# Kernel tuning notes

Hardware: AMD Instinct MI355X
Metric: run time of the kernel (lower is better)

Reference implementation:

```python
import jax, jax.numpy as jnp
import numpy as np
from jax import lax

DN = ('NCHW', 'OIHW', 'NCHW')


def conv3x3(x, w, groups=1):
    return lax.conv_general_dilated(x, w, window_strides=(1, 1),
                                    padding=((1, 1), (1, 1)),
                                    dimension_numbers=DN,
                                    feature_group_count=groups)


def conv1x1(x, w):
    return lax.conv_general_dilated(x, w, window_strides=(1, 1),
                                    padding=((0, 0), (0, 0)),
                                    dimension_numbers=DN)


def l2_normalize(t, eps=1e-12):
    n = jnp.sqrt(jnp.sum(t * t, axis=-1, keepdims=True))
    return t / jnp.maximum(n, eps)


def setup_inputs() -> dict:
    key = jax.random.key(0)
    ks = jax.random.split(key, 10)
    B, C, H, W = 4, 64, 256, 256
    heads = 8
    s = 0.05
    return {
        'x': jax.random.normal(ks[0], (B, C, H, W), jnp.float32),
        'w_iem': jax.random.normal(ks[1], (C, C, 3, 3), jnp.float32) * s,
        'w_nem': jax.random.normal(ks[2], (C, C, 3, 3), jnp.float32) * s,
        'w_iem_dw': jax.random.normal(ks[3], (C, 1, 3, 3), jnp.float32) * s,
        'w_nem_dw': jax.random.normal(ks[4], (C, 1, 3, 3), jnp.float32) * s,
        'w_q': jax.random.normal(ks[5], (C, C, 1, 1), jnp.float32) * s,
        'w_k': jax.random.normal(ks[6], (C, C, 1, 1), jnp.float32) * s,
        'w_v': jax.random.normal(ks[7], (C, C, 1, 1), jnp.float32) * s,
        'w_proj': jax.random.normal(ks[8], (C, C, 1, 1), jnp.float32) * s,
        'temperature': jnp.ones((1, heads, 1, 1, 1, 1), jnp.float32),
    }


def igam_forward(x, w_iem, w_nem, w_iem_dw, w_nem_dw, w_q, w_k, w_v, w_proj,
                 temperature, num_heads=8, window_size=8):
    b, c, h, w = x.shape
    ws = window_size
    pad_h = (ws - h % ws) % ws
    pad_w = (ws - w % ws) % ws
    if pad_h or pad_w:  # replicate pad on right/bottom (static)
        x = jnp.pad(x, ((0, 0), (0, 0), (0, pad_h), (0, pad_w)), mode='edge')
    hp, wp = x.shape[-2:]
    heads = num_heads
    d = c // heads
    nh, nw = hp // ws, wp // ws

    illumination_map = conv3x3(jax.nn.sigmoid(conv3x3(x, w_iem)), w_iem_dw, groups=c)
    noise_map = conv3x3(jax.nn.sigmoid(conv3x3(x, w_nem)), w_nem_dw, groups=c)
    illum_scalar = jnp.mean(illumination_map, axis=1, keepdims=True)  # (b,1,hp,wp)
    noise_scalar = jnp.mean(noise_map, axis=1, keepdims=True)

    q = conv1x1(illumination_map, w_q)
    k = conv1x1(noise_map, w_k)
    v = conv1x1(x, w_v)

    def to_windows(t):  # (b,c,hp,wp) -> (b,heads,nh,nw,ws*ws,d)
        t = t.reshape(b, heads, d, hp, wp).transpose(0, 1, 3, 4, 2)
        t = t.reshape(b, heads, nh, ws, nw, ws, d).transpose(0, 1, 2, 4, 3, 5, 6)
        return t.reshape(b, heads, nh, nw, ws * ws, d)

    def scalar_to_windows(t):  # (b,1,hp,wp) -> (b,1,nh,nw,ws*ws,1)
        t = t.reshape(b, 1, nh, ws, nw, ws).transpose(0, 1, 2, 4, 3, 5)
        return t.reshape(b, 1, nh, nw, ws * ws, 1)

    qw = l2_normalize(to_windows(q)) * (1.0 + scalar_to_windows(illum_scalar))
    kw = l2_normalize(to_windows(k)) * jnp.clip(1.0 - scalar_to_windows(noise_scalar), 0.0, 1.0)
    vw = to_windows(v)

    scale = d ** (-0.5)
    attn = jnp.einsum('bhnmqd,bhnmkd->bhnmqk', qw, kw) * scale * temperature
    attn = jax.nn.softmax(attn, axis=-1)
    outw = jnp.einsum('bhnmqk,bhnmkd->bhnmqd', attn, vw)

    # merge windows back to (b, c, hp, wp)
    outw = outw.reshape(b, heads, nh, nw, ws, ws, d).transpose(0, 1, 6, 2, 4, 3, 5)
    out = outw.reshape(b, heads * d, nh * ws, nw * ws)
    if pad_h or pad_w:
        out = out[:, :, :h, :w]
    return conv1x1(out, w_proj)


def reference(x, w_iem, w_nem, w_iem_dw, w_nem_dw, w_q, w_k, w_v, w_proj,
              temperature):
    return igam_forward(x, w_iem, w_nem, w_iem_dw, w_nem_dw, w_q, w_k, w_v,
                        w_proj, temperature)
```

## Files before the change

kernel.cpp:

```cpp
#include <hip/hip_runtime.h>
#include <math.h>

#define W_ 256
#define H_ 256
#define HW 65536
#define CC 64

typedef _Float16 h16;
typedef _Float16 half8 __attribute__((ext_vector_type(8)));
typedef float f32x4  __attribute__((ext_vector_type(4)));
typedef float f32x16 __attribute__((ext_vector_type(16)));

__device__ __forceinline__ unsigned pk2(float a, float b) {
  union { h16 h[2]; unsigned u; } c;
  c.h[0] = (h16)a; c.h[1] = (h16)b;
  return c.u;
}
__device__ __forceinline__ void plswap(unsigned &a, unsigned &b) {
  asm volatile("v_permlane32_swap_b32 %0, %1" : "+v"(a), "+v"(b));
}

__global__ __launch_bounds__(256) void k_wprep(
    const float* __restrict__ wi, const float* __restrict__ wn, h16* __restrict__ Bt)
{
  int i = blockIdx.x * 256 + threadIdx.x;
  if (i >= 128 * 576) return;
  int co = i / 576, k = i - co * 576;
  int tap = k >> 6, ci = k & 63;
  const float* src = (co < 64) ? wi : wn;
  int c = co & 63;
  Bt[i] = (h16)src[(c * 64 + ci) * 9 + tap];
}

__global__ __launch_bounds__(256) void k_wprep2(
    const float* __restrict__ wq, const float* __restrict__ wk,
    const float* __restrict__ wv, const float* __restrict__ wp,
    const float* __restrict__ wdw1, const float* __restrict__ wdw2,
    h16* __restrict__ W)
{
  int i = blockIdx.x * 256 + threadIdx.x;
  if (i >= 17536) return;
  if (i < 16384) {
    int m = i >> 12, e = i & 4095;
    const float* s = (m == 0) ? wq : (m == 1) ? wk : (m == 2) ? wv : wp;
    W[i] = (h16)s[e];
  } else {
    int e = i - 16384;
    int pass = e / 576, rem = e - pass * 576;
    int tap = rem >> 6, c = rem & 63;
    const float* s = pass ? wdw2 : wdw1;
    W[i] = (h16)s[c * 9 + tap];
  }
}

__global__ __launch_bounds__(256) void k_xpose(
    const float* __restrict__ x, h16* __restrict__ xT)
{
  __shared__ __align__(16) char sm[64 * 132];
  const int tid = threadIdx.x;
  const int xt = blockIdx.x, y = blockIdx.y, b = blockIdx.z;
  const int x0 = xt * 64;
  const float* xb = x + ((size_t)b * CC) * HW + y * W_ + x0;
  const int ci = tid >> 2, q = tid & 3;
#pragma unroll
  for (int k = 0; k < 4; ++k) {
    const int pc = q + k * 4;
    float4 v = *(const float4*)(xb + (size_t)ci * HW + pc * 4);
    const int px = pc * 4;
    *(h16*)(sm + (px + 0) * 132 + ci * 2) = (h16)v.x;
    *(h16*)(sm + (px + 1) * 132 + ci * 2) = (h16)v.y;
    *(h16*)(sm + (px + 2) * 132 + ci * 2) = (h16)v.z;
    *(h16*)(sm + (px + 3) * 132 + ci * 2) = (h16)v.w;
  }
  __syncthreads();
  h16* dst = xT + (((size_t)b * 256 + y) * 256 + x0) * 64;
#pragma unroll
  for (int it = 0; it < 2; ++it) {
    int task = tid + it * 256;
    int px = task >> 3, c8 = task & 7;
    int4 d = *(const int4*)(sm + px * 132 + c8 * 16);
    *(int4*)(dst + px * 64 + c8 * 8) = d;
  }
}

__global__ __launch_bounds__(512) void k_conv3x3x2(
    const h16* __restrict__ xT, const h16* __restrict__ Bt,
    h16* __restrict__ T1, h16* __restrict__ T2)
{
  __shared__ __align__(16) char lds[38016];

  const int tid = threadIdx.x;
  const int b = blockIdx.z, ry = blockIdx.y, cx = blockIdx.x;
  const int y0 = ry * 2, x0 = cx * 64;

  {
    const h16* xb = xT + ((size_t)b * 256) * 256 * 64;
    int4 zero4; zero4.x = zero4.y = zero4.z = zero4.w = 0;
#pragma unroll
    for (int it = 0; it < 5; ++it) {
      int idx = tid + it * 512;
      if (idx < 2112) {
        int pxr = idx >> 3, c8 = idx & 7;
        int r = pxr / 66, c = pxr - r * 66;
        int gy = y0 - 1 + r, gx = x0 - 1 + c;
        int4 d = zero4;
        if ((unsigned)gy < 256u && (unsigned)gx < 256u)
          d = *(const int4*)(xb + ((size_t)(gy * 256 + gx)) * 64 + c8 * 8);
        *(int4*)(lds + pxr * 144 + c8 * 16) = d;
      }
    }
  }
  __syncthreads();

  const int wv = tid >> 6, lane = tid & 63;
  const int wn_ = wv & 3;
  const int wm_ = wv >> 2;
  const int cob = wn_ * 32;
  const int pxb = wm_ * 64;
  const int lg = lane >> 4, lr = lane & 15;

  const char* pB[4];
#pragma unroll
  for (int pi = 0; pi < 4; ++pi) {
    int opx = (pxb + pi * 16 + lr) & 63;
    pB[pi] = lds + (wm_ * 66 + opx) * 144 + lg * 16;
  }
  const h16* wb0 = Bt + (size_t)(cob + lr) * 576 + lg * 8;
  const h16* wb1 = wb0 + 16 * 576;

  f32x4 acc[2][4];
#pragma unroll
  for (int i = 0; i < 2; ++i)
#pragma unroll
    for (int j = 0; j < 4; ++j) acc[i][j] = (f32x4){0.f, 0.f, 0.f, 0.f};

#pragma unroll
  for (int tap = 0; tap < 9; ++tap) {
    const int dy = tap / 3, dx = tap - dy * 3;
#pragma unroll
    for (int kh = 0; kh < 2; ++kh) {
      const int loff = (dy * 66 + dx) * 144 + kh * 64;
      const int koff = tap * 64 + kh * 32;
      half8 a0 = *(const half8*)(wb0 + koff);
      half8 a1 = *(const half8*)(wb1 + koff);
      half8 b0 = *(const half8*)(pB[0] + loff);
      half8 b1 = *(const half8*)(pB[1] + loff);
      half8 b2 = *(const half8*)(pB[2] + loff);
      half8 b3 = *(const half8*)(pB[3] + loff);
      acc[0][0] = __builtin_amdgcn_mfma_f32_16x16x32_f16(a0, b0, acc[0][0], 0, 0, 0);
      acc[0][1] = __builtin_amdgcn_mfma_f32_16x16x32_f16(a0, b1, acc[0][1], 0, 0, 0);
      acc[0][2] = __builtin_amdgcn_mfma_f32_16x16x32_f16(a0, b2, acc[0][2], 0, 0, 0);
      acc[0][3] = __builtin_amdgcn_mfma_f32_16x16x32_f16(a0, b3, acc[0][3], 0, 0, 0);
      acc[1][0] = __builtin_amdgcn_mfma_f32_16x16x32_f16(a1, b0, acc[1][0], 0, 0, 0);
      acc[1][1] = __builtin_amdgcn_mfma_f32_16x16x32_f16(a1, b1, acc[1][1], 0, 0, 0);
      acc[1][2] = __builtin_amdgcn_mfma_f32_16x16x32_f16(a1, b2, acc[1][2], 0, 0, 0);
      acc[1][3] = __builtin_amdgcn_mfma_f32_16x16x32_f16(a1, b3, acc[1][3], 0, 0, 0);
    }
  }
  __syncthreads();

#pragma unroll
  for (int ni = 0; ni < 2; ++ni) {
#pragma unroll
    for (int pi = 0; pi < 4; ++pi) {
      const int opx = (pxb + pi * 16 + lr) & 63;
      const int pxid = wm_ * 64 + opx;
      const int co = cob + ni * 16 + lg * 4;
      float s0 = 1.f / (1.f + __expf(-acc[ni][pi][0]));
      float s1 = 1.f / (1.f + __expf(-acc[ni][pi][1]));
      float s2 = 1.f / (1.f + __expf(-acc[ni][pi][2]));
      float s3 = 1.f / (1.f + __expf(-acc[ni][pi][3]));
      uint2 d; d.x = pk2(s0, s1); d.y = pk2(s2, s3);
      *(uint2*)(lds + pxid * 272 + co * 2) = d;
    }
  }
  __syncthreads();

  {
    int px = tid >> 3, chg = tid & 7;
#pragma unroll
    for (int seg = 0; seg < 4; ++seg) {
      int t = seg >> 1, rr = seg & 1;
      int4 d = *(const int4*)(lds + (rr * 64 + px) * 272 + t * 128 + chg * 16);
      h16* dst = (t ? T2 : T1) + (((size_t)b * 256 + (y0 + rr)) * 256 + (x0 + px)) * 64 + chg * 8;
      *(int4*)dst = d;
    }
  }
}

#define HALO 0
#define DWW  14400
#define SIN  16704
#define INA  17216
#define INB  26432
#define INC  35648

__global__ __launch_bounds__(512, 6) void k_megaattn(
    const h16* __restrict__ T1g, const h16* __restrict__ T2g,
    const h16* __restrict__ xT, const h16* __restrict__ Wall,
    const float* __restrict__ temp, float* __restrict__ out)
{
  __shared__ __align__(16) char sm[44864];
  const int tid = threadIdx.x;
  const int wv = tid >> 6, lane = tid & 63;
  const int lg = lane >> 4, lr = lane & 15;
  const int wn = wv & 3;
  const int wm = wv >> 2;

  const int u = blockIdx.x;
  const int xcd = u & 7, idx = u >> 3;
  const int flat = xcd * 512 + idx;
  const int b = flat >> 10, rem = flat & 1023;
  const int wy = rem >> 5, wx = rem & 31;
  const int y0 = wy * 8, x0 = wx * 8;

  half8 wf[4][2];
#pragma unroll
  for (int m = 0; m < 4; ++m)
#pragma unroll
    for (int ks = 0; ks < 2; ++ks)
      wf[m][ks] = *(const half8*)(Wall + m * 4096 + (wn * 16 + lr) * 64 + ks * 32 + lg * 8);
  const float thv = temp[wn * 2 + (lg >> 1)];

  int4 zero4; zero4.x = zero4.y = zero4.z = zero4.w = 0;
  int4 h1r[2], h2r[2], xtr;
#pragma unroll
  for (int i = 0; i < 2; ++i) {
    int cc = tid + i * 512;
    bool act = cc < 800;
    int prow = act ? (cc >> 3) : 0;
    int c8 = cc & 7;
    int hy = prow / 10, hx = prow - hy * 10;
    int gy = y0 - 1 + hy, gx = x0 - 1 + hx;
    bool ok = act && (unsigned)gy < 256u && (unsigned)gx < 256u;
    size_t ga = (((size_t)b * 256 + gy) * 256 + gx) * (size_t)64 + c8 * 8;
    h1r[i] = ok ? *(const int4*)(T1g + ga) : zero4;
    h2r[i] = ok ? *(const int4*)(T2g + ga) : zero4;
  }
  const size_t wbase = (((size_t)b * 256 + y0) * 256 + x0) * 64;
  xtr = *(const int4*)(xT + wbase + (size_t)(tid >> 6) * 16384 + (tid & 63) * 8);

#pragma unroll
  for (int i = 0; i < 2; ++i) {
    int cc = tid + i * 512;
    if (cc < 800) *(int4*)(sm + HALO + (cc >> 3) * 144 + (cc & 7) * 16) = h1r[i];
  }
  if (tid < 144) {
    int4 d = *(const int4*)(Wall + 16384 + tid * 8);
    *(int4*)(sm + DWW + tid * 16) = d;
  }
  __syncthreads();

  const half8 hz8 = {(h16)0, (h16)0, (h16)0, (h16)0, (h16)0, (h16)0, (h16)0, (h16)0};
#pragma unroll
  for (int pass = 0; pass < 2; ++pass) {
    const int outb = pass ? INB : INA;
    {
      const int px = tid >> 3, c8 = tid & 7;
      const int py = px >> 3, pxx = px & 7;
      half8 af = hz8;
#pragma unroll
      for (int tap = 0; tap < 9; ++tap) {
        const int dy = tap / 3, dx = tap - dy * 3;
        half8 v  = *(const half8*)(sm + HALO + ((py + dy) * 10 + pxx + dx) * 144 + c8 * 16);
        half8 w8 = *(const half8*)(sm + DWW + pass * 1152 + tap * 128 + c8 * 16);
        af += v * w8;
      }
      *(half8*)(sm + outb + px * 144 + c8 * 16) = af;
      float s = 0.f;
#pragma unroll
      for (int j = 0; j < 8; ++j) s += (float)af[j];
      s += __shfl_xor(s, 1);
      s += __shfl_xor(s, 2);
      s += __shfl_xor(s, 4);
      if (c8 == 0) *(float*)(sm + SIN + pass * 256 + px * 4) = s * (1.f / 64.f);
    }
    __syncthreads();
    if (pass == 0) {
#pragma unroll
      for (int i = 0; i < 2; ++i) {
        int cc = tid + i * 512;
        if (cc < 800) *(int4*)(sm + HALO + (cc >> 3) * 144 + (cc & 7) * 16) = h2r[i];
      }
      __syncthreads();
    }
  }

  {
    int py = tid >> 6, off = tid & 63;
    int px = py * 8 + (off >> 3);
    *(int4*)(sm + INC + px * 144 + (off & 7) * 16) = xtr;
  }
  __syncthreads();

  f32x4 aq[2], ak[2], av[2];
#pragma unroll
  for (int pi = 0; pi < 2; ++pi) {
    aq[pi] = (f32x4){0.f, 0.f, 0.f, 0.f};
    ak[pi] = (f32x4){0.f, 0.f, 0.f, 0.f};
    av[pi] = (f32x4){0.f, 0.f, 0.f, 0.f};
  }
  __builtin_amdgcn_s_setprio(1);
#pragma unroll
  for (int pi = 0; pi < 2; ++pi)
#pragma unroll
    for (int ks = 0; ks < 2; ++ks) {
      const int boff = (wm * 32 + pi * 16 + lr) * 144 + ks * 64 + lg * 16;
      half8 b0 = *(const half8*)(sm + INA + boff);
      half8 b1 = *(const half8*)(sm + INB + boff);
      half8 b2 = *(const half8*)(sm + INC + boff);
      aq[pi] = __builtin_amdgcn_mfma_f32_16x16x32_f16(wf[0][ks], b0, aq[pi], 0, 0, 0);
      ak[pi] = __builtin_amdgcn_mfma_f32_16x16x32_f16(wf[1][ks], b1, ak[pi], 0, 0, 0);
      av[pi] = __builtin_amdgcn_mfma_f32_16x16x32_f16(wf[2][ks], b2, av[pi], 0, 0, 0);
    }
  __builtin_amdgcn_s_setprio(0);
  __syncthreads();

#pragma unroll
  for (int pi = 0; pi < 2; ++pi) {
    const int px = wm * 32 + pi * 16 + lr;
    const float si = *(const float*)(sm + SIN + px * 4);
    const float sn = *(const float*)(sm + SIN + 256 + px * 4);
    float s2 = aq[pi][0]*aq[pi][0] + aq[pi][1]*aq[pi][1] + aq[pi][2]*aq[pi][2] + aq[pi][3]*aq[pi][3];
    float qs = (1.f + si) * (0.35355339059327373f * 1.4426950408889634f) * thv /
               fmaxf(sqrtf(s2 + __shfl_xor(s2, 16)), 1e-12f);
    float k2 = ak[pi][0]*ak[pi][0] + ak[pi][1]*ak[pi][1] + ak[pi][2]*ak[pi][2] + ak[pi][3]*ak[pi][3];
    float ks2 = fminf(fmaxf(1.f - sn, 0.f), 1.f) /
                fmaxf(sqrtf(k2 + __shfl_xor(k2, 16)), 1e-12f);
    uint2 dq; dq.x = pk2(aq[pi][0]*qs, aq[pi][1]*qs); dq.y = pk2(aq[pi][2]*qs, aq[pi][3]*qs);
    uint2 dk; dk.x = pk2(ak[pi][0]*ks2, ak[pi][1]*ks2); dk.y = pk2(ak[pi][2]*ks2, ak[pi][3]*ks2);
    *(uint2*)(sm + INA + px * 144 + (wn * 16 + lg * 4) * 2) = dq;
    *(uint2*)(sm + INB + px * 144 + (wn * 16 + lg * 4) * 2) = dk;
#pragma unroll
    for (int r = 0; r < 4; ++r)
      *(h16*)(sm + INC + (wn * 16 + lg * 4 + r) * 144 + px * 2) = (h16)av[pi][r];
  }
  __syncthreads();

  const int l31 = lane & 31, hi = lane >> 5;
  const half8 hz = hz8;
  const f32x16 z16 = {0.f,0.f,0.f,0.f,0.f,0.f,0.f,0.f,0.f,0.f,0.f,0.f,0.f,0.f,0.f,0.f};
  {
    const int h = wv;
    half8 kfr[2], qfr[2];
#pragma unroll
    for (int kt = 0; kt < 2; ++kt)
      kfr[kt] = hi ? hz : *(const half8*)(sm + INB + (kt * 32 + l31) * 144 + h * 16);
#pragma unroll
    for (int qt = 0; qt < 2; ++qt)
      qfr[qt] = hi ? hz : *(const half8*)(sm + INA + (qt * 32 + l31) * 144 + h * 16);

#pragma unroll
    for (int qt = 0; qt < 2; ++qt) {
      __builtin_amdgcn_s_setprio(1);
      f32x16 s0 = __builtin_amdgcn_mfma_f32_32x32x16_f16(kfr[0], qfr[qt], z16, 0, 0, 0);
      f32x16 s1 = __builtin_amdgcn_mfma_f32_32x32x16_f16(kfr[1], qfr[qt], z16, 0, 0, 0);
      __builtin_amdgcn_s_setprio(0);
      float sum = 0.f;
#pragma unroll
      for (int i = 0; i < 16; ++i) { s0[i] = __builtin_amdgcn_exp2f(s0[i]); sum += s0[i]; }
#pragma unroll
      for (int i = 0; i < 16; ++i) { s1[i] = __builtin_amdgcn_exp2f(s1[i]); sum += s1[i]; }
      sum += __shfl_xor(sum, 32);
      const float inv = 1.f / sum;

      half8 pa[4];
#pragma unroll
      for (int st = 0; st < 4; ++st) {
        const int rb = (st & 1) * 8;
        float p0, p1, p2, p3, p4, p5, p6, p7;
        if (st < 2) {
          p0 = s0[rb+0]; p1 = s0[rb+1]; p2 = s0[rb+2]; p3 = s0[rb+3];
          p4 = s0[rb+4]; p5 = s0[rb+5]; p6 = s0[rb+6]; p7 = s0[rb+7];
        } else {
          p0 = s1[rb+0]; p1 = s1[rb+1]; p2 = s1[rb+2]; p3 = s1[rb+3];
          p4 = s1[rb+4]; p5 = s1[rb+5]; p6 = s1[rb+6]; p7 = s1[rb+7];
        }
        unsigned x0_ = pk2(p0, p1), x1_ = pk2(p2, p3);
        unsigned y0_ = pk2(p4, p5), y1_ = pk2(p6, p7);
        plswap(x0_, y0_);
        plswap(x1_, y1_);
        union { unsigned uu4[4]; half8 h; } uu;
        uu.uu4[0] = x0_; uu.uu4[1] = x1_; uu.uu4[2] = y0_; uu.uu4[3] = y1_;
        pa[st] = uu.h;
      }
      f32x16 oacc = z16;
      __builtin_amdgcn_s_setprio(1);
#pragma unroll
      for (int st = 0; st < 4; ++st) {
        half8 vfr = (l31 < 8)
          ? *(const half8*)(sm + INC + (h * 8 + l31) * 144 + (st * 16 + hi * 8) * 2)
          : hz;
        oacc = __builtin_amdgcn_mfma_f32_32x32x16_f16(vfr, pa[st], oacc, 0, 0, 0);
      }
      __builtin_amdgcn_s_setprio(0);
      {
        uint2 dAO;
        dAO.x = pk2(oacc[0] * inv, oacc[1] * inv);
        dAO.y = pk2(oacc[2] * inv, oacc[3] * inv);
        *(uint2*)(sm + INA + (qt * 32 + l31) * 144 + (h * 8 + 4 * hi) * 2) = dAO;
      }
    }
  }
  __syncthreads();

  f32x4 pacc[2];
#pragma unroll
  for (int pi = 0; pi < 2; ++pi) pacc[pi] = (f32x4){0.f, 0.f, 0.f, 0.f};
  __builtin_amdgcn_s_setprio(1);
#pragma unroll
  for (int pi = 0; pi < 2; ++pi)
#pragma unroll
    for (int ks = 0; ks < 2; ++ks) {
      half8 bfr = *(const half8*)(sm + INA + (wm * 32 + pi * 16 + lr) * 144 + ks * 64 + lg * 16);
      pacc[pi] = __builtin_amdgcn_mfma_f32_16x16x32_f16(wf[3][ks], bfr, pacc[pi], 0, 0, 0);
    }
  __builtin_amdgcn_s_setprio(0);
#pragma unroll
  for (int pi = 0; pi < 2; ++pi) {
    const int px = wm * 32 + pi * 16 + lr;
    const int py = px >> 3, pxx = px & 7;
    const int co = wn * 16 + lg * 4;
    float* ob = out + ((size_t)(b * CC + co)) * HW + (size_t)(y0 + py) * W_ + (x0 + pxx);
    ob[0]      = pacc[pi][0];
    ob[HW]     = pacc[pi][1];
    ob[2 * HW] = pacc[pi][2];
    ob[3 * HW] = pacc[pi][3];
  }
}

extern "C" void kernel_launch(void* const* d_in, const int* in_sizes, int n_in,
                              void* d_out, int out_size, void* d_ws, size_t ws_size,
                              hipStream_t stream) {
  const float* x        = (const float*)d_in[0];
  const float* w_iem    = (const float*)d_in[1];
  const float* w_nem    = (const float*)d_in[2];
  const float* w_iem_dw = (const float*)d_in[3];
  const float* w_nem_dw = (const float*)d_in[4];
  const float* w_q      = (const float*)d_in[5];
  const float* w_k      = (const float*)d_in[6];
  const float* w_v      = (const float*)d_in[7];
  const float* w_proj   = (const float*)d_in[8];
  const float* temp     = (const float*)d_in[9];
  float* outp = (float*)d_out;

  const size_t PLE = (size_t)4 * CC * HW;
  h16* h0   = (h16*)d_ws;
  h16* T1   = h0;
  h16* T2   = h0 + PLE;
  h16* xT   = h0 + 2 * PLE;
  h16* Bt   = h0 + 3 * PLE;
  h16* Wall = Bt + 73728;

  dim3 b256(256), b512(512);

  k_wprep    <<<dim3(288),        b256, 0, stream>>>(w_iem, w_nem, Bt);
  k_wprep2   <<<dim3(69),         b256, 0, stream>>>(w_q, w_k, w_v, w_proj,
                                                     w_iem_dw, w_nem_dw, Wall);
  k_xpose    <<<dim3(4, 256, 4),  b256, 0, stream>>>(x, xT);
  k_conv3x3x2<<<dim3(4, 128, 4),  b512, 0, stream>>>(xT, Bt, T1, T2);
  k_megaattn <<<dim3(4096),       b512, 0, stream>>>(T1, T2, xT, Wall, temp, outp);
}
```

Before: 192.1 us.

## Enlarge conv3x3 tile to four rows and 64 channels per wave

The fused dual 3x3 conv kernel now computes four output rows per block instead of two. Each wave covers 64 output channels by 64 pixels, so every loaded B fragment feeds four MFMAs and halo reloads per output shrink. In exchange, LDS grows to about 68KB, accumulator registers double, and there are half as many blocks. Separately, the attention kernel writes the x tile into LDS earlier, which removes one barrier.

Result: slower. 206.1 us (+7.3%).

```diff
diff --git a/kernel.cpp b/kernel.cpp
--- a/kernel.cpp
+++ b/kernel.cpp
@@ -83,23 +83,23 @@
   }
 }
 
-__global__ __launch_bounds__(512) void k_conv3x3x2(
+__global__ __launch_bounds__(512, 4) void k_conv3x3x2(
     const h16* __restrict__ xT, const h16* __restrict__ Bt,
     h16* __restrict__ T1, h16* __restrict__ T2)
 {
-  __shared__ __align__(16) char lds[38016];
+  __shared__ __align__(16) char lds[69632];
 
   const int tid = threadIdx.x;
   const int b = blockIdx.z, ry = blockIdx.y, cx = blockIdx.x;
-  const int y0 = ry * 2, x0 = cx * 64;
+  const int y0 = ry * 4, x0 = cx * 64;
 
   {
     const h16* xb = xT + ((size_t)b * 256) * 256 * 64;
     int4 zero4; zero4.x = zero4.y = zero4.z = zero4.w = 0;
 #pragma unroll
-    for (int it = 0; it < 5; ++it) {
+    for (int it = 0; it < 7; ++it) {
       int idx = tid + it * 512;
-      if (idx < 2112) {
+      if (idx < 3168) {
         int pxr = idx >> 3, c8 = idx & 7;
         int r = pxr / 66, c = pxr - r * 66;
         int gy = y0 - 1 + r, gx = x0 - 1 + c;
@@ -113,24 +113,20 @@
   __syncthreads();
 
   const int wv = tid >> 6, lane = tid & 63;
-  const int wn_ = wv & 3;
-  const int wm_ = wv >> 2;
-  const int cob = wn_ * 32;
-  const int pxb = wm_ * 64;
+  const int wn_ = wv & 1;
+  const int wm_ = wv >> 1;
+  const int cob = wn_ * 64;
   const int lg = lane >> 4, lr = lane & 15;
 
   const char* pB[4];
 #pragma unroll
-  for (int pi = 0; pi < 4; ++pi) {
-    int opx = (pxb + pi * 16 + lr) & 63;
-    pB[pi] = lds + (wm_ * 66 + opx) * 144 + lg * 16;
-  }
-  const h16* wb0 = Bt + (size_t)(cob + lr) * 576 + lg * 8;
-  const h16* wb1 = wb0 + 16 * 576;
-
-  f32x4 acc[2][4];
-#pragma unroll
-  for (int i = 0; i < 2; ++i)
+  for (int pi = 0; pi < 4; ++pi)
+    pB[pi] = lds + (wm_ * 66 + pi * 16 + lr) * 144 + lg * 16;
+  const h16* wbb = Bt + (size_t)(cob + lr) * 576 + lg * 8;
+
+  f32x4 acc[4][4];
+#pragma unroll
+  for (int i = 0; i < 4; ++i)
 #pragma unroll
     for (int j = 0; j < 4; ++j) acc[i][j] = (f32x4){0.f, 0.f, 0.f, 0.f};
 
@@ -141,30 +137,27 @@
     for (int kh = 0; kh < 2; ++kh) {
       const int loff = (dy * 66 + dx) * 144 + kh * 64;
       const int koff = tap * 64 + kh * 32;
-      half8 a0 = *(const half8*)(wb0 + koff);
-      half8 a1 = *(const half8*)(wb1 + koff);
-      half8 b0 = *(const half8*)(pB[0] + loff);
-      half8 b1 = *(const half8*)(pB[1] + loff);
-      half8 b2 = *(const half8*)(pB[2] + loff);
-      half8 b3 = *(const half8*)(pB[3] + loff);
-      acc[0][0] = __builtin_amdgcn_mfma_f32_16x16x32_f16(a0, b0, acc[0][0], 0, 0, 0);
-      acc[0][1] = __builtin_amdgcn_mfma_f32_16x16x32_f16(a0, b1, acc[0][1], 0, 0, 0);
-      acc[0][2] = __builtin_amdgcn_mfma_f32_16x16x32_f16(a0, b2, acc[0][2], 0, 0, 0);
-      acc[0][3] = __builtin_amdgcn_mfma_f32_16x16x32_f16(a0, b3, acc[0][3], 0, 0, 0);
-      acc[1][0] = __builtin_amdgcn_mfma_f32_16x16x32_f16(a1, b0, acc[1][0], 0, 0, 0);
-      acc[1][1] = __builtin_amdgcn_mfma_f32_16x16x32_f16(a1, b1, acc[1][1], 0, 0, 0);
-      acc[1][2] = __builtin_amdgcn_mfma_f32_16x16x32_f16(a1, b2, acc[1][2], 0, 0, 0);
-      acc[1][3] = __builtin_amdgcn_mfma_f32_16x16x32_f16(a1, b3, acc[1][3], 0, 0, 0);
-    }
-  }
-  __syncthreads();
-
-#pragma unroll
-  for (int ni = 0; ni < 2; ++ni) {
+      half8 a0 = *(const half8*)(wbb + 0 * 16 * 576 + koff);
+      half8 a1 = *(const half8*)(wbb + 1 * 16 * 576 + koff);
+      half8 a2 = *(const half8*)(wbb + 2 * 16 * 576 + koff);
+      half8 a3 = *(const half8*)(wbb + 3 * 16 * 576 + koff);
+#pragma unroll
+      for (int pi = 0; pi < 4; ++pi) {
+        half8 bfr = *(const half8*)(pB[pi] + loff);
+        acc[0][pi] = __builtin_amdgcn_mfma_f32_16x16x32_f16(a0, bfr, acc[0][pi], 0, 0, 0);
+        acc[1][pi] = __builtin_amdgcn_mfma_f32_16x16x32_f16(a1, bfr, acc[1][pi], 0, 0, 0);
+        acc[2][pi] = __builtin_amdgcn_mfma_f32_16x16x32_f16(a2, bfr, acc[2][pi], 0, 0, 0);
+        acc[3][pi] = __builtin_amdgcn_mfma_f32_16x16x32_f16(a3, bfr, acc[3][pi], 0, 0, 0);
+      }
+    }
+  }
+  __syncthreads();
+
+#pragma unroll
+  for (int ni = 0; ni < 4; ++ni) {
 #pragma unroll
     for (int pi = 0; pi < 4; ++pi) {
-      const int opx = (pxb + pi * 16 + lr) & 63;
-      const int pxid = wm_ * 64 + opx;
+      const int pxid = wm_ * 64 + pi * 16 + lr;
       const int co = cob + ni * 16 + lg * 4;
       float s0 = 1.f / (1.f + __expf(-acc[ni][pi][0]));
       float s1 = 1.f / (1.f + __expf(-acc[ni][pi][1]));
@@ -177,12 +170,12 @@
   __syncthreads();
 
   {
-    int px = tid >> 3, chg = tid & 7;
-#pragma unroll
-    for (int seg = 0; seg < 4; ++seg) {
-      int t = seg >> 1, rr = seg & 1;
-      int4 d = *(const int4*)(lds + (rr * 64 + px) * 272 + t * 128 + chg * 16);
-      h16* dst = (t ? T2 : T1) + (((size_t)b * 256 + (y0 + rr)) * 256 + (x0 + px)) * 64 + chg * 8;
+    int pxq = tid >> 3, chg = tid & 7;
+#pragma unroll
+    for (int seg = 0; seg < 8; ++seg) {
+      int t = seg >> 2, rr = seg & 3;
+      int4 d = *(const int4*)(lds + (rr * 64 + pxq) * 272 + t * 128 + chg * 16);
+      h16* dst = (t ? T2 : T1) + (((size_t)b * 256 + (y0 + rr)) * 256 + (x0 + pxq)) * 64 + chg * 8;
       *(int4*)dst = d;
     }
   }
@@ -245,6 +238,11 @@
     int cc = tid + i * 512;
     if (cc < 800) *(int4*)(sm + HALO + (cc >> 3) * 144 + (cc & 7) * 16) = h1r[i];
   }
+  {
+    int py = tid >> 6, off = tid & 63;
+    int px = py * 8 + (off >> 3);
+    *(int4*)(sm + INC + px * 144 + (off & 7) * 16) = xtr;
+  }
   if (tid < 144) {
     int4 d = *(const int4*)(Wall + 16384 + tid * 8);
     *(int4*)(sm + DWW + tid * 16) = d;
@@ -285,13 +283,6 @@
       __syncthreads();
     }
   }
-
-  {
-    int py = tid >> 6, off = tid & 63;
-    int px = py * 8 + (off >> 3);
-    *(int4*)(sm + INC + px * 144 + (off & 7) * 16) = xtr;
-  }
-  __syncthreads();
 
   f32x4 aq[2], ak[2], av[2];
 #pragma unroll
@@ -458,6 +449,6 @@
   k_wprep2   <<<dim3(69),         b256, 0, stream>>>(w_q, w_k, w_v, w_proj,
                                                      w_iem_dw, w_nem_dw, Wall);
   k_xpose    <<<dim3(4, 256, 4),  b256, 0, stream>>>(x, xT);
-  k_conv3x3x2<<<dim3(4, 128, 4),  b512, 0, stream>>>(xT, Bt, T1, T2);
+  k_conv3x3x2<<<dim3(4, 64, 4),   b512, 0, stream>>>(xT, Bt, T1, T2);
   k_megaattn <<<dim3(4096),       b512, 0, stream>>>(T1, T2, xT, Wall, temp, outp);
 }
```
